# Optimization experiments

Hardware: AMD Instinct MI355X
Metric: run time of the kernel (lower is better)

## Reference

```python
import jax, jax.numpy as jnp
import numpy as np

THRESHOLD = 0.05
STRIDE = (1, 1)
PADDING = ((1, 1), (1, 1))


def ternary_quantize(w, threshold=THRESHOLD):
    # w -> {-1, 0, +1}; zero where |w| <= threshold
    mask = (jnp.abs(w) > threshold).astype(w.dtype)
    return jnp.sign(w) * mask


def setup_inputs() -> dict:
    key = jax.random.key(0)
    k1, k2 = jax.random.split(key)
    B, Cin, H, W = 32, 256, 56, 56
    Cout, kH, kW = 256, 3, 3
    fan_in = Cin * kH * kW
    std = np.sqrt(2.0 / fan_in) * 2.0
    x = jax.random.normal(k1, (B, Cin, H, W), dtype=jnp.float32)
    weight = jax.random.normal(k2, (Cout, Cin, kH, kW), dtype=jnp.float32) * std
    bias = jnp.zeros((Cout,), dtype=jnp.float32)
    return {"x": x, "weight": weight, "bias": bias}


def reference(x, weight, bias):
    w_t = ternary_quantize(weight, THRESHOLD)
    out = jax.lax.conv_general_dilated(
        x, w_t,
        window_strides=STRIDE,
        padding=PADDING,
        dimension_numbers=("NCHW", "OIHW", "NCHW"),
    )
    return out + bias[None, :, None, None]
```

## Files before the change

### kernel.cpp

```cpp
#include <hip/hip_runtime.h>

#define CIN   256
#define COUT  256
#define HH    56
#define WW    56
#define BATCH 32
#define KTOT  2304
#define HP    58
#define WP    58
#define NPIX  (BATCH*HH*WW)
#define HWSZ  (HH*WW)

typedef __bf16 bf16x8 __attribute__((ext_vector_type(8)));
typedef float  f32x4  __attribute__((ext_vector_type(4)));

#define AS1 __attribute__((address_space(1)))
#define AS3 __attribute__((address_space(3)))

__device__ __forceinline__ unsigned short f2bf(float f) {
  union { float f; unsigned int u; } v; v.f = f;
  unsigned int u = v.u;
  u += 0x7fffu + ((u >> 16) & 1u);
  return (unsigned short)(u >> 16);
}

__device__ __forceinline__ void async16(const void* g, void* l) {
  __builtin_amdgcn_global_load_lds((const AS1 unsigned int*)g,
                                   (AS3 unsigned int*)l, 16, 0, 0);
}

__global__ __launch_bounds__(256) void quant_w(const float* __restrict__ w,
                                               unsigned short* __restrict__ wr) {
  int tid = blockIdx.x * 256 + threadIdx.x;
  if (tid >= COUT * KTOT) return;
  int co  = tid / KTOT;
  int rem = tid - co * KTOT;
  int tap = rem >> 8;
  int ci  = rem & 255;
  int kh  = tap / 3;
  int kw  = tap - kh * 3;
  float v = w[((co * CIN + ci) * 3 + kh) * 3 + kw];
  float q = (fabsf(v) > 0.05f) ? ((v > 0.f) ? 1.f : -1.f) : 0.f;
  wr[tid] = f2bf(q);
}

#define TSTR 60
__global__ __launch_bounds__(256) void pad_nhwc(const float* __restrict__ x,
                                                unsigned short* __restrict__ xp) {
  const int nhp = blockIdx.x;
  const int n   = nhp / HP;
  const int hp  = nhp - n * HP;
  const int ci0 = blockIdx.y * 64;
  const int t   = threadIdx.x;
  const size_t obase = (size_t)nhp * (WP * 256);

  __shared__ __align__(16) float tile[64 * TSTR];
  const bool hborder = (hp == 0) || (hp == HP - 1);

  if (!hborder) {
    const int h = hp - 1;
    #pragma unroll
    for (int it = 0; it < 4; ++it) {
      int linear = it * 256 + t;
      if (linear < 896) {
        int cil = linear / 14;
        int w4  = linear - cil * 14;
        *(float4*)&tile[cil * TSTR + w4 * 4] =
            *(const float4*)&x[(((size_t)(n * CIN + ci0 + cil)) * HH + h) * WW + w4 * 4];
      }
    }
  }
  __syncthreads();

  #pragma unroll
  for (int it = 0; it < 2; ++it) {
    int linear = it * 256 + t;
    if (linear < 464) {
      int wp = linear >> 3;
      int g  = linear & 7;
      unsigned int pk[4] = {0u, 0u, 0u, 0u};
      if (!hborder && wp != 0 && wp != WP - 1) {
        #pragma unroll
        for (int j = 0; j < 4; ++j) {
          unsigned int lo = f2bf(tile[(g * 8 + 2 * j) * TSTR + (wp - 1)]);
          unsigned int hi = f2bf(tile[(g * 8 + 2 * j + 1) * TSTR + (wp - 1)]);
          pk[j] = lo | (hi << 16);
        }
      }
      uint4 v; v.x = pk[0]; v.y = pk[1]; v.z = pk[2]; v.w = pk[3];
      *(uint4*)(xp + obase + (size_t)wp * 256 + ci0 + g * 8) = v;
    }
  }
}


#define NOWAIT (void)0
#define VM4 asm volatile("s_waitcnt vmcnt(4)" ::: "memory")
#define VM0 asm volatile("s_waitcnt vmcnt(0)" ::: "memory")

#define STAGE4(buf_, kn_) do {                                                \
  const int kn__ = (kn_);                                                     \
  const size_t koW_ = (size_t)kn__ << 5;                                      \
  const int tap_ = kn__ >> 3;                                                 \
  const int kh_  = tap_ / 3;                                                  \
  const int kw_  = tap_ - kh_ * 3;                                            \
  const size_t koX_ = (size_t)((kh_ * WP + kw_) * 256 + ((kn__ & 7) << 5));   \
  char* da_ = smem + (buf_) * 8192 + t * 16;                                  \
  char* db_ = smem + 24576 + (buf_) * 8192 + t * 16;                          \
  async16(Wr + koW_ + aSrc0, da_);                                            \
  async16(Wr + koW_ + aSrc1, da_ + 4096);                                     \
  async16(Xp + koX_ + bSrc0, db_);                                            \
  async16(Xp + koX_ + bSrc1, db_ + 4096);                                     \
} while (0)

#define PHASE(buf_, WAITE, ...) do {                                          \
  __VA_ARGS__;                                                                \
  bf16x8 af_[4], bf_[4];                                                      \
  _Pragma("unroll")                                                           \
  for (int mt = 0; mt < 4; ++mt)                                              \
    af_[mt] = *(const bf16x8*)(smem + (buf_) * 8192 + rdA + mt * 1024);       \
  _Pragma("unroll")                                                           \
  for (int nt = 0; nt < 4; ++nt)                                              \
    bf_[nt] = *(const bf16x8*)(smem + 24576 + (buf_) * 8192 + rdB + nt * 1024);\
  __builtin_amdgcn_s_barrier();                                               \
  asm volatile("s_waitcnt lgkmcnt(0)" ::: "memory");                          \
  __builtin_amdgcn_sched_barrier(0);                                          \
  __builtin_amdgcn_s_setprio(1);                                              \
  _Pragma("unroll")                                                           \
  for (int mt = 0; mt < 4; ++mt)                                              \
    _Pragma("unroll")                                                         \
    for (int nt = 0; nt < 4; ++nt)                                            \
      acc[mt][nt] = __builtin_amdgcn_mfma_f32_16x16x32_bf16(                  \
          af_[mt], bf_[nt], acc[mt][nt], 0, 0, 0);                            \
  __builtin_amdgcn_s_setprio(0);                                              \
  WAITE;                                                                      \
  __builtin_amdgcn_s_barrier();                                               \
} while (0)

__global__ __launch_bounds__(256, 3) void conv_gemm(
    const unsigned short* __restrict__ Wr,
    const unsigned short* __restrict__ Xp,
    const float* __restrict__ bias,
    float* __restrict__ out) {
  extern __shared__ char smem[];

  const int t    = threadIdx.x;
  const int lane = t & 63;
  const int wv   = t >> 6;
  const int wm   = wv >> 1;
  const int wn   = wv & 1;
  const int l15  = lane & 15;
  const int quad = lane >> 4;

  const int bid = blockIdx.x;
  const int nf  = (bid & 7) * 196 + (bid >> 3);
  const int cob = nf & 1;
  const int pb  = nf >> 1;
  const int co0 = cob * 128;
  const int p0  = pb * 128;

  const int srow = t >> 2;
  const int schk = (t & 3) ^ ((srow >> 1) & 3);

  const size_t aSrc0 = (size_t)(co0 + srow) * KTOT + schk * 8;
  const size_t aSrc1 = aSrc0 + (size_t)64 * KTOT;

  const int pA = p0 + srow;
  const int pB = pA + 64;
  const int nA = pA / HWSZ;  const int hwA = pA - nA * HWSZ;
  const int hA = hwA / WW;   const int wA  = hwA - hA * WW;
  const int nB = pB / HWSZ;  const int hwB = pB - nB * HWSZ;
  const int hB = hwB / WW;   const int wB  = hwB - hB * WW;
  const size_t bSrc0 = ((size_t)((nA * HP + hA) * WP + wA)) * 256 + schk * 8;
  const size_t bSrc1 = ((size_t)((nB * HP + hB) * WP + wB)) * 256 + schk * 8;

  const int rchk = (quad ^ ((l15 >> 1) & 3)) * 16;
  const int rdA  = (wm * 64 + l15) * 64 + rchk;
  const int rdB  = (wn * 64 + l15) * 64 + rchk;

  f32x4 acc[4][4];
  #pragma unroll
  for (int i = 0; i < 4; ++i)
    #pragma unroll
    for (int j = 0; j < 4; ++j)
      acc[i][j] = (f32x4){0.f, 0.f, 0.f, 0.f};

  STAGE4(0, 0);
  STAGE4(1, 1);
  VM4;
  __builtin_amdgcn_s_barrier();

  #pragma unroll 1
  for (int it = 0; it < 23; ++it) {
    const int k0 = 3 * it;
    PHASE(0, VM4, STAGE4(2, k0 + 2));
    PHASE(1, VM4, STAGE4(0, k0 + 3));
    PHASE(2, VM4, STAGE4(1, k0 + 4));
  }
  PHASE(0, VM4, STAGE4(2, 71));
  PHASE(1, VM0, NOWAIT);
  PHASE(2, NOWAIT, NOWAIT);

  float bv[4][4];
  #pragma unroll
  for (int mt = 0; mt < 4; ++mt)
    #pragma unroll
    for (int r = 0; r < 4; ++r)
      bv[mt][r] = bias[co0 + wm * 64 + mt * 16 + quad * 4 + r];

  #pragma unroll
  for (int nt = 0; nt < 4; ++nt) {
    const int p  = p0 + wn * 64 + nt * 16 + l15;
    const int np = p / HWSZ;
    const int hw = p - np * HWSZ;
    const size_t obase = (size_t)np * (COUT * HWSZ) + hw;
    #pragma unroll
    for (int mt = 0; mt < 4; ++mt) {
      const int co = co0 + wm * 64 + mt * 16 + quad * 4;
      #pragma unroll
      for (int r = 0; r < 4; ++r)
        out[obase + (size_t)(co + r) * HWSZ] = acc[mt][nt][r] + bv[mt][r];
    }
  }
}

extern "C" void kernel_launch(void* const* d_in, const int* in_sizes, int n_in,
                              void* d_out, int out_size, void* d_ws, size_t ws_size,
                              hipStream_t stream) {
  const float* x    = (const float*)d_in[0];
  const float* w    = (const float*)d_in[1];
  const float* bias = (const float*)d_in[2];
  float* out        = (float*)d_out;

  unsigned short* xp = (unsigned short*)d_ws;
  unsigned short* wr = (unsigned short*)((char*)d_ws + 55115776);

  quant_w<<<dim3((COUT * KTOT) / 256), dim3(256), 0, stream>>>(w, wr);
  pad_nhwc<<<dim3(BATCH * HP, 4), dim3(256), 0, stream>>>(x, xp);

  (void)hipFuncSetAttribute((const void*)conv_gemm,
                            hipFuncAttributeMaxDynamicSharedMemorySize, 49152);
  conv_gemm<<<dim3(1568), dim3(256), 49152, stream>>>(wr, xp, bias, out);
}
```

Before: 331.9 us.

## Enlarge conv GEMM tile to all 256 Cout by 224 pixels and fuse prep kernels

Each conv_gemm block now uses 512 threads to compute all 256 output channels for a 224-pixel tile, with a 4x7 MFMA accumulator grid per wave and 96KB of triple-buffered LDS. The aim is to stop re-reading the same pixel data for two Cout halves and to raise MFMA work per LDS load. The weight quantization and padding kernels are merged into one launch, and the padding pack loop is rotated to spread LDS bank accesses. The trade-offs are high register pressure (112 accumulator registers), at most one block per CU given the LDS size, only 448 blocks (an uneven number of waves across CUs), and extra unused pixel rows staged past the end of the tile.

```diff
diff --git a/kernel.cpp b/kernel.cpp
--- a/kernel.cpp
+++ b/kernel.cpp
@@ -10,6 +10,8 @@
 #define WP    58
 #define NPIX  (BATCH*HH*WW)
 #define HWSZ  (HH*WW)
+#define BN    224
+#define NBLK  (NPIX/BN)
 
 typedef __bf16 bf16x8 __attribute__((ext_vector_type(8)));
 typedef float  f32x4  __attribute__((ext_vector_type(4)));
@@ -29,28 +31,31 @@
                                    (AS3 unsigned int*)l, 16, 0, 0);
 }
 
-__global__ __launch_bounds__(256) void quant_w(const float* __restrict__ w,
-                                               unsigned short* __restrict__ wr) {
-  int tid = blockIdx.x * 256 + threadIdx.x;
-  if (tid >= COUT * KTOT) return;
-  int co  = tid / KTOT;
-  int rem = tid - co * KTOT;
-  int tap = rem >> 8;
-  int ci  = rem & 255;
-  int kh  = tap / 3;
-  int kw  = tap - kh * 3;
-  float v = w[((co * CIN + ci) * 3 + kh) * 3 + kw];
-  float q = (fabsf(v) > 0.05f) ? ((v > 0.f) ? 1.f : -1.f) : 0.f;
-  wr[tid] = f2bf(q);
-}
-
 #define TSTR 60
-__global__ __launch_bounds__(256) void pad_nhwc(const float* __restrict__ x,
-                                                unsigned short* __restrict__ xp) {
-  const int nhp = blockIdx.x;
+#define QBLKS 2304
+__global__ __launch_bounds__(256) void prep(const float* __restrict__ w,
+                                            unsigned short* __restrict__ wr,
+                                            const float* __restrict__ x,
+                                            unsigned short* __restrict__ xp) {
+  const int bx = blockIdx.x;
+  if (bx < QBLKS) {
+    int tid = bx * 256 + threadIdx.x;
+    int co  = tid / KTOT;
+    int rem = tid - co * KTOT;
+    int tap = rem >> 8;
+    int ci  = rem & 255;
+    int kh  = tap / 3;
+    int kw  = tap - kh * 3;
+    float v = w[((co * CIN + ci) * 3 + kh) * 3 + kw];
+    float q = (fabsf(v) > 0.05f) ? ((v > 0.f) ? 1.f : -1.f) : 0.f;
+    wr[tid] = f2bf(q);
+    return;
+  }
+  const int pbx = bx - QBLKS;
+  const int nhp = pbx >> 2;
   const int n   = nhp / HP;
   const int hp  = nhp - n * HP;
-  const int ci0 = blockIdx.y * 64;
+  const int ci0 = (pbx & 3) << 6;
   const int t   = threadIdx.x;
   const size_t obase = (size_t)nhp * (WP * 256);
 
@@ -82,9 +87,10 @@
       if (!hborder && wp != 0 && wp != WP - 1) {
         #pragma unroll
         for (int j = 0; j < 4; ++j) {
-          unsigned int lo = f2bf(tile[(g * 8 + 2 * j) * TSTR + (wp - 1)]);
-          unsigned int hi = f2bf(tile[(g * 8 + 2 * j + 1) * TSTR + (wp - 1)]);
-          pk[j] = lo | (hi << 16);
+          int jr = (j + g) & 3;
+          unsigned int lo = f2bf(tile[(g * 8 + 2 * jr) * TSTR + (wp - 1)]);
+          unsigned int hi = f2bf(tile[(g * 8 + 2 * jr + 1) * TSTR + (wp - 1)]);
+          pk[jr] = lo | (hi << 16);
         }
       }
       uint4 v; v.x = pk[0]; v.y = pk[1]; v.z = pk[2]; v.w = pk[3];
@@ -105,23 +111,23 @@
   const int kh_  = tap_ / 3;                                                  \
   const int kw_  = tap_ - kh_ * 3;                                            \
   const size_t koX_ = (size_t)((kh_ * WP + kw_) * 256 + ((kn__ & 7) << 5));   \
-  char* da_ = smem + (buf_) * 8192 + t * 16;                                  \
-  char* db_ = smem + 24576 + (buf_) * 8192 + t * 16;                          \
+  char* da_ = smem + (buf_) * 32768 + t * 16;                                 \
+  char* db_ = smem + (buf_) * 32768 + 16384 + t * 16;                         \
   async16(Wr + koW_ + aSrc0, da_);                                            \
-  async16(Wr + koW_ + aSrc1, da_ + 4096);                                     \
+  async16(Wr + koW_ + aSrc1, da_ + 8192);                                     \
   async16(Xp + koX_ + bSrc0, db_);                                            \
-  async16(Xp + koX_ + bSrc1, db_ + 4096);                                     \
+  async16(Xp + koX_ + bSrc1, db_ + 8192);                                     \
 } while (0)
 
 #define PHASE(buf_, WAITE, ...) do {                                          \
   __VA_ARGS__;                                                                \
-  bf16x8 af_[4], bf_[4];                                                      \
+  bf16x8 af_[4], bf_[7];                                                      \
   _Pragma("unroll")                                                           \
   for (int mt = 0; mt < 4; ++mt)                                              \
-    af_[mt] = *(const bf16x8*)(smem + (buf_) * 8192 + rdA + mt * 1024);       \
+    af_[mt] = *(const bf16x8*)(smem + (buf_) * 32768 + rdA + mt * 1024);      \
   _Pragma("unroll")                                                           \
-  for (int nt = 0; nt < 4; ++nt)                                              \
-    bf_[nt] = *(const bf16x8*)(smem + 24576 + (buf_) * 8192 + rdB + nt * 1024);\
+  for (int nt = 0; nt < 7; ++nt)                                              \
+    bf_[nt] = *(const bf16x8*)(smem + (buf_) * 32768 + 16384 + rdB + nt * 1024);\
   __builtin_amdgcn_s_barrier();                                               \
   asm volatile("s_waitcnt lgkmcnt(0)" ::: "memory");                          \
   __builtin_amdgcn_sched_barrier(0);                                          \
@@ -129,7 +135,7 @@
   _Pragma("unroll")                                                           \
   for (int mt = 0; mt < 4; ++mt)                                              \
     _Pragma("unroll")                                                         \
-    for (int nt = 0; nt < 4; ++nt)                                            \
+    for (int nt = 0; nt < 7; ++nt)                                            \
       acc[mt][nt] = __builtin_amdgcn_mfma_f32_16x16x32_bf16(                  \
           af_[mt], bf_[nt], acc[mt][nt], 0, 0, 0);                            \
   __builtin_amdgcn_s_setprio(0);                                              \
@@ -137,7 +143,7 @@
   __builtin_amdgcn_s_barrier();                                               \
 } while (0)
 
-__global__ __launch_bounds__(256, 3) void conv_gemm(
+__global__ __launch_bounds__(512, 2) void conv_gemm(
     const unsigned short* __restrict__ Wr,
     const unsigned short* __restrict__ Xp,
     const float* __restrict__ bias,
@@ -153,20 +159,17 @@
   const int quad = lane >> 4;
 
   const int bid = blockIdx.x;
-  const int nf  = (bid & 7) * 196 + (bid >> 3);
-  const int cob = nf & 1;
-  const int pb  = nf >> 1;
-  const int co0 = cob * 128;
-  const int p0  = pb * 128;
+  const int pb  = (bid & 7) * 56 + (bid >> 3);
+  const int p0  = pb * BN;
 
   const int srow = t >> 2;
   const int schk = (t & 3) ^ ((srow >> 1) & 3);
 
-  const size_t aSrc0 = (size_t)(co0 + srow) * KTOT + schk * 8;
-  const size_t aSrc1 = aSrc0 + (size_t)64 * KTOT;
+  const size_t aSrc0 = (size_t)srow * KTOT + schk * 8;
+  const size_t aSrc1 = aSrc0 + (size_t)128 * KTOT;
 
   const int pA = p0 + srow;
-  const int pB = pA + 64;
+  const int pB = pA + 128;
   const int nA = pA / HWSZ;  const int hwA = pA - nA * HWSZ;
   const int hA = hwA / WW;   const int wA  = hwA - hA * WW;
   const int nB = pB / HWSZ;  const int hwB = pB - nB * HWSZ;
@@ -175,14 +178,14 @@
   const size_t bSrc1 = ((size_t)((nB * HP + hB) * WP + wB)) * 256 + schk * 8;
 
   const int rchk = (quad ^ ((l15 >> 1) & 3)) * 16;
-  const int rdA  = (wm * 64 + l15) * 64 + rchk;
-  const int rdB  = (wn * 64 + l15) * 64 + rchk;
-
-  f32x4 acc[4][4];
+  const int rdA  = (wm * 64  + l15) * 64 + rchk;
+  const int rdB  = (wn * 112 + l15) * 64 + rchk;
+
+  f32x4 acc[4][7];
   #pragma unroll
   for (int i = 0; i < 4; ++i)
     #pragma unroll
-    for (int j = 0; j < 4; ++j)
+    for (int j = 0; j < 7; ++j)
       acc[i][j] = (f32x4){0.f, 0.f, 0.f, 0.f};
 
   STAGE4(0, 0);
@@ -206,17 +209,17 @@
   for (int mt = 0; mt < 4; ++mt)
     #pragma unroll
     for (int r = 0; r < 4; ++r)
-      bv[mt][r] = bias[co0 + wm * 64 + mt * 16 + quad * 4 + r];
-
-  #pragma unroll
-  for (int nt = 0; nt < 4; ++nt) {
-    const int p  = p0 + wn * 64 + nt * 16 + l15;
+      bv[mt][r] = bias[wm * 64 + mt * 16 + quad * 4 + r];
+
+  #pragma unroll
+  for (int nt = 0; nt < 7; ++nt) {
+    const int p  = p0 + wn * 112 + nt * 16 + l15;
     const int np = p / HWSZ;
     const int hw = p - np * HWSZ;
     const size_t obase = (size_t)np * (COUT * HWSZ) + hw;
     #pragma unroll
     for (int mt = 0; mt < 4; ++mt) {
-      const int co = co0 + wm * 64 + mt * 16 + quad * 4;
+      const int co = wm * 64 + mt * 16 + quad * 4;
       #pragma unroll
       for (int r = 0; r < 4; ++r)
         out[obase + (size_t)(co + r) * HWSZ] = acc[mt][nt][r] + bv[mt][r];
@@ -235,10 +238,9 @@
   unsigned short* xp = (unsigned short*)d_ws;
   unsigned short* wr = (unsigned short*)((char*)d_ws + 55115776);
 
-  quant_w<<<dim3((COUT * KTOT) / 256), dim3(256), 0, stream>>>(w, wr);
-  pad_nhwc<<<dim3(BATCH * HP, 4), dim3(256), 0, stream>>>(x, xp);
+  prep<<<dim3(QBLKS + BATCH * HP * 4), dim3(256), 0, stream>>>(w, wr, x, xp);
 
   (void)hipFuncSetAttribute((const void*)conv_gemm,
-                            hipFuncAttributeMaxDynamicSharedMemorySize, 49152);
-  conv_gemm<<<dim3(1568), dim3(256), 49152, stream>>>(wr, xp, bias, out);
-}
+                            hipFuncAttributeMaxDynamicSharedMemorySize, 98304);
+  conv_gemm<<<dim3(NBLK), dim3(512), 98304, stream>>>(wr, xp, bias, out);
+}
```

Result: faster. 324.1 us (-2.3%).
